# Kernel optimization log

Measured on AMD Instinct MI355X. Metric: run time of the kernel, lower is better.

Reference implementation:

```python
import jax, jax.numpy as jnp
import numpy as np

B, K, N, F, H = 20000, 10, 100000, 256, 128


def setup_inputs() -> dict:
    key = jax.random.key(0)
    ks = jax.random.split(key, 8)
    neighbors = jax.random.randint(ks[0], (B, K), 0, N)
    embed_table = jax.random.normal(ks[1], (N, F), dtype=jnp.float32)
    w = lambda k, shp: jax.random.normal(k, shp, dtype=jnp.float32) * 0.05
    return {
        "neighbors": neighbors,
        "embed_table": embed_table,
        "W1a": w(ks[2], (F, H)), "W1b": w(ks[3], (H, H)),
        "W2a": w(ks[4], (F, H)), "W2b": w(ks[5], (H, H)),
        "W3a": w(ks[6], (F, H)), "W3b": w(ks[7], (H, H)),
    }


def reference(neighbors, embed_table, W1a, W1b, W2a, W2b, W3a, W3b):
    # Gather each batch node's K sampled neighbor embeddings: [B, K, F]
    x = embed_table[neighbors]
    # Three MLP projections: Linear(F,H,no bias) -> tanh -> Linear(H,H,no bias)
    q = jnp.tanh(x @ W1a) @ W1b              # [B, K, H]  (att1)
    k = jnp.tanh(x @ W2a) @ W2b              # [B, K, H]  (att2)
    v = jnp.tanh(x @ W3a) @ W3b              # [B, K, H]  (att3)
    # Per-node attention over the K neighbors, softmax along last dim
    att = jax.nn.softmax(jnp.einsum('bid,bjd->bij', q, k), axis=-1)  # [B, K, K]
    # torch: sum over rows of (att @ v) -> contract both i and j
    out = jnp.einsum('bij,bjd->bd', att, v)  # [B, H]
    return out
```

## Files before the change

### kernel.cpp

```cpp
#include <hip/hip_runtime.h>
#include <hip/hip_bf16.h>

constexpr int B_ = 20000;
constexpr int K_ = 10;
constexpr int N_ = 100000;
constexpr int F_ = 256;
constexpr int H_ = 128;
constexpr int RW = 3 * H_;

typedef __attribute__((ext_vector_type(8))) short bf16x8;
typedef __attribute__((ext_vector_type(4))) float f32x4;

__device__ __forceinline__ unsigned short f2bf(float x) {
  unsigned int u = __builtin_bit_cast(unsigned int, x);
  unsigned int r = u + 0x7fffu + ((u >> 16) & 1u);
  return (unsigned short)(r >> 16);
}

__device__ __forceinline__ float bf2f(unsigned int u16) {
  return __builtin_bit_cast(float, u16 << 16);
}

__device__ __forceinline__ unsigned int cvt_pk_bf16(float lo, float hi) {
  unsigned int r;
  asm("v_cvt_pk_bf16_f32 %0, %1, %2" : "=v"(r) : "v"(lo), "v"(hi));
  return r;
}

__device__ __forceinline__ float fast_tanh(float x) {
  float e = __expf(2.0f * x);
  return 1.0f - 2.0f * __builtin_amdgcn_rcpf(e + 1.0f);
}

__global__ __launch_bounds__(256) void prep_kernel(
    const float* __restrict__ W1a, const float* __restrict__ W1b,
    const float* __restrict__ W2a, const float* __restrict__ W2b,
    const float* __restrict__ W3a, const float* __restrict__ W3b,
    unsigned short* __restrict__ wat2, unsigned short* __restrict__ wbt2) {
  const float* Wa[3] = {W1a, W2a, W3a};
  const float* Wb[3] = {W1b, W2b, W3b};
  int g = blockIdx.x * 256 + threadIdx.x;
  if (g < 3 * 64 * 512) {
    int chunk = g >> 9;
    int e = g & 511;
    int lane = e >> 3, j = e & 7;
    int c = chunk & 7;
    int ks = (chunk >> 3) & 7;
    int p = chunk >> 6;
    int k = 32 * ks + 8 * (lane >> 4) + j;
    int h = 16 * c + (lane & 15);
    wat2[g] = f2bf(Wa[p][k * H_ + h]);
  } else {
    int g2 = g - 3 * 64 * 512;
    int chunk = g2 >> 9;
    int e = g2 & 511;
    int lane = e >> 3, j = e & 7;
    int ks2 = chunk & 3;
    int c2 = (chunk >> 2) & 7;
    int p = chunk >> 5;
    int k = 32 * ks2 + 8 * (lane >> 4) + j;
    int h2 = 16 * c2 + (lane & 15);
    wbt2[g2] = f2bf(Wb[p][k * H_ + h2]);
  }
}

constexpr int MT = 16;
constexpr int XS = F_ + 8;
constexpr int TS = H_ + 8;

__global__ __launch_bounds__(128) void proj_kernel(
    const float* __restrict__ E,
    const unsigned short* __restrict__ wat2,
    const unsigned short* __restrict__ wbt2,
    unsigned short* __restrict__ qkvI) {
  __shared__ unsigned short xs[MT * XS];
  __shared__ unsigned short ts[MT * TS];

  const int tid = threadIdx.x;
  const int lane = tid & 63;
  const int w = tid >> 6;
  const int l15 = lane & 15;
  const int q = lane >> 4;
  const int row0 = blockIdx.x * MT;

  {
    const float4* Eg = (const float4*)E;
#pragma unroll
    for (int it = 0; it < 8; ++it) {
      int i = tid + 128 * it;
      int r = i >> 6;
      int c4 = i & 63;
      int row = row0 + r;
      if (row >= N_) row = N_ - 1;
      float4 v = Eg[(size_t)row * (F_ / 4) + c4];
      unsigned int lo = cvt_pk_bf16(v.x, v.y);
      unsigned int hi = cvt_pk_bf16(v.z, v.w);
      *(uint2*)&xs[r * XS + c4 * 4] = make_uint2(lo, hi);
    }
  }
  __syncthreads();

  for (int p = 0; p < 3; ++p) {
    const unsigned short* __restrict__ wa = wat2 + p * (64 * 512);
    const unsigned short* __restrict__ wb = wbt2 + p * (32 * 512);

    f32x4 acc[4];
#pragma unroll
    for (int i = 0; i < 4; ++i) acc[i] = (f32x4)0.0f;

#pragma unroll
    for (int ks = 0; ks < 8; ++ks) {
      bf16x8 bx = *(const bf16x8*)&xs[l15 * XS + 32 * ks + 8 * q];
#pragma unroll
      for (int i = 0; i < 4; ++i) {
        bf16x8 af = *(const bf16x8*)&wa[(ks * 8 + 4 * w + i) * 512 + lane * 8];
        acc[i] = __builtin_amdgcn_mfma_f32_16x16x32_bf16(af, bx, acc[i], 0, 0, 0);
      }
    }

    __syncthreads();
#pragma unroll
    for (int i = 0; i < 4; ++i) {
      unsigned int lo = cvt_pk_bf16(fast_tanh(acc[i][0]), fast_tanh(acc[i][1]));
      unsigned int hi = cvt_pk_bf16(fast_tanh(acc[i][2]), fast_tanh(acc[i][3]));
      *(uint2*)&ts[l15 * TS + 16 * (4 * w + i) + 4 * q] = make_uint2(lo, hi);
    }
    __syncthreads();

    f32x4 ac2[4];
#pragma unroll
    for (int i = 0; i < 4; ++i) ac2[i] = (f32x4)0.0f;

#pragma unroll
    for (int ks2 = 0; ks2 < 4; ++ks2) {
      bf16x8 bt = *(const bf16x8*)&ts[l15 * TS + 32 * ks2 + 8 * q];
#pragma unroll
      for (int i = 0; i < 4; ++i) {
        bf16x8 ab = *(const bf16x8*)&wb[((4 * w + i) * 4 + ks2) * 512 + lane * 8];
        ac2[i] = __builtin_amdgcn_mfma_f32_16x16x32_bf16(ab, bt, ac2[i], 0, 0, 0);
      }
    }

#pragma unroll
    for (int i = 0; i < 4; ++i) {
      int n = row0 + l15;
      if (n < N_) {
        unsigned int lo = cvt_pk_bf16(ac2[i][0], ac2[i][1]);
        unsigned int hi = cvt_pk_bf16(ac2[i][2], ac2[i][3]);
        *(uint2*)&qkvI[(size_t)n * RW + p * H_ + 16 * (4 * w + i) + 4 * q] =
            make_uint2(lo, hi);
      }
    }
  }
}

__global__ __launch_bounds__(256) void agg_kernel(
    const int* __restrict__ nbr,
    const unsigned short* __restrict__ qkvI,
    float* __restrict__ out) {
  const int lane = threadIdx.x & 63;
  const int wv = threadIdx.x >> 6;
  const int b = blockIdx.x * 4 + wv;
  const int l15 = lane & 15;
  const int kg = lane >> 4;

  const int ni = nbr[b * K_ + (l15 < K_ ? l15 : 0)];
  const size_t nbase = (size_t)ni * RW;

  f32x4 sc = (f32x4)0.0f;
#pragma unroll
  for (int k = 0; k < 4; ++k) {
    const int off = k * 32 + kg * 8;
    bf16x8 qf = *(const bf16x8*)&qkvI[nbase + off];
    bf16x8 kf = *(const bf16x8*)&qkvI[nbase + H_ + off];
    sc = __builtin_amdgcn_mfma_f32_16x16x32_bf16(qf, kf, sc, 0, 0, 0);
  }

  if (l15 >= K_) {
#pragma unroll
    for (int r = 0; r < 4; ++r) sc[r] = -3.0e38f;
  }

  float mx[4], e[4], sm[4];
#pragma unroll
  for (int r = 0; r < 4; ++r) mx[r] = sc[r];
#pragma unroll
  for (int st = 1; st < 16; st <<= 1)
#pragma unroll
    for (int r = 0; r < 4; ++r) mx[r] = fmaxf(mx[r], __shfl_xor(mx[r], st, 16));
#pragma unroll
  for (int r = 0; r < 4; ++r) { e[r] = __expf(sc[r] - mx[r]); sm[r] = e[r]; }
#pragma unroll
  for (int st = 1; st < 16; st <<= 1)
#pragma unroll
    for (int r = 0; r < 4; ++r) sm[r] += __shfl_xor(sm[r], st, 16);

  float cs = 0.0f;
#pragma unroll
  for (int r = 0; r < 4; ++r) {
    float a = e[r] * __builtin_amdgcn_rcpf(sm[r]);
    if (kg * 4 + r >= K_) a = 0.0f;
    cs += a;
  }
  cs += __shfl_xor(cs, 16, 64);
  cs += __shfl_xor(cs, 32, 64);

  float o0 = 0.0f, o1 = 0.0f;
#pragma unroll
  for (int j = 0; j < K_; ++j) {
    const float cj = __shfl(cs, j, 64);
    const int nj = __shfl(ni, j, 64);
    const unsigned int v2 =
        *(const unsigned int*)&qkvI[(size_t)nj * RW + 2 * H_ + 2 * lane];
    o0 = fmaf(cj, bf2f(v2 & 0xffffu), o0);
    o1 = fmaf(cj, bf2f(v2 >> 16), o1);
  }
  *(float2*)&out[(size_t)b * H_ + 2 * lane] = make_float2(o0, o1);
}

extern "C" void kernel_launch(void* const* d_in, const int* in_sizes, int n_in,
                              void* d_out, int out_size, void* d_ws, size_t ws_size,
                              hipStream_t stream) {
  const int* nbr = (const int*)d_in[0];
  const float* E = (const float*)d_in[1];
  const float* W1a = (const float*)d_in[2];
  const float* W1b = (const float*)d_in[3];
  const float* W2a = (const float*)d_in[4];
  const float* W2b = (const float*)d_in[5];
  const float* W3a = (const float*)d_in[6];
  const float* W3b = (const float*)d_in[7];
  float* out = (float*)d_out;

  unsigned short* qkvI = (unsigned short*)d_ws;
  unsigned short* wat2 = qkvI + (size_t)N_ * RW;
  unsigned short* wbt2 = wat2 + (size_t)3 * 64 * 512;

  prep_kernel<<<(3 * 64 * 512 + 3 * 32 * 512) / 256, 256, 0, stream>>>(
      W1a, W1b, W2a, W2b, W3a, W3b, wat2, wbt2);
  proj_kernel<<<(N_ + MT - 1) / MT, 128, 0, stream>>>(E, wat2, wbt2, qkvI);
  agg_kernel<<<B_ / 4, 256, 0, stream>>>(nbr, qkvI, out);
}
```

Baseline: 262.0 us.

## Tile projection over 64 rows with per-wave row ownership and private scratch

The projection kernel now handles 64 embedding rows per block with 256 threads. Each wave owns 16 rows and computes all 128 output columns, instead of two waves splitting the columns of a 16-row tile. The tanh intermediate goes to a per-wave LDS scratch, so the block-wide barriers between the two matmuls are removed. Weight fragments are reused across more rows per block, at the cost of more accumulator registers and larger LDS use, which may lower occupancy.

```diff
diff --git a/kernel.cpp b/kernel.cpp
--- a/kernel.cpp
+++ b/kernel.cpp
@@ -64,17 +64,17 @@
   }
 }
 
-constexpr int MT = 16;
+constexpr int MT = 64;
 constexpr int XS = F_ + 8;
-constexpr int TS = H_ + 8;
-
-__global__ __launch_bounds__(128) void proj_kernel(
+constexpr int SPAD = 68;
+
+__global__ __launch_bounds__(256) void proj_kernel(
     const float* __restrict__ E,
     const unsigned short* __restrict__ wat2,
     const unsigned short* __restrict__ wbt2,
     unsigned short* __restrict__ qkvI) {
   __shared__ unsigned short xs[MT * XS];
-  __shared__ unsigned short ts[MT * TS];
+  __shared__ unsigned int scr[4 * 16 * SPAD];
 
   const int tid = threadIdx.x;
   const int lane = tid & 63;
@@ -82,12 +82,13 @@
   const int l15 = lane & 15;
   const int q = lane >> 4;
   const int row0 = blockIdx.x * MT;
+  unsigned int* scw = scr + w * (16 * SPAD);
 
   {
     const float4* Eg = (const float4*)E;
 #pragma unroll
-    for (int it = 0; it < 8; ++it) {
-      int i = tid + 128 * it;
+    for (int it = 0; it < 16; ++it) {
+      int i = tid + 256 * it;
       int r = i >> 6;
       int c4 = i & 63;
       int row = row0 + r;
@@ -104,50 +105,48 @@
     const unsigned short* __restrict__ wa = wat2 + p * (64 * 512);
     const unsigned short* __restrict__ wb = wbt2 + p * (32 * 512);
 
-    f32x4 acc[4];
-#pragma unroll
-    for (int i = 0; i < 4; ++i) acc[i] = (f32x4)0.0f;
+    f32x4 acc[8];
+#pragma unroll
+    for (int hp = 0; hp < 8; ++hp) acc[hp] = (f32x4)0.0f;
 
 #pragma unroll
     for (int ks = 0; ks < 8; ++ks) {
-      bf16x8 bx = *(const bf16x8*)&xs[l15 * XS + 32 * ks + 8 * q];
-#pragma unroll
-      for (int i = 0; i < 4; ++i) {
-        bf16x8 af = *(const bf16x8*)&wa[(ks * 8 + 4 * w + i) * 512 + lane * 8];
-        acc[i] = __builtin_amdgcn_mfma_f32_16x16x32_bf16(af, bx, acc[i], 0, 0, 0);
+      bf16x8 bx = *(const bf16x8*)&xs[(16 * w + l15) * XS + 32 * ks + 8 * q];
+#pragma unroll
+      for (int hp = 0; hp < 8; ++hp) {
+        bf16x8 af = *(const bf16x8*)&wa[(ks * 8 + hp) * 512 + lane * 8];
+        acc[hp] = __builtin_amdgcn_mfma_f32_16x16x32_bf16(af, bx, acc[hp], 0, 0, 0);
       }
     }
 
-    __syncthreads();
-#pragma unroll
-    for (int i = 0; i < 4; ++i) {
-      unsigned int lo = cvt_pk_bf16(fast_tanh(acc[i][0]), fast_tanh(acc[i][1]));
-      unsigned int hi = cvt_pk_bf16(fast_tanh(acc[i][2]), fast_tanh(acc[i][3]));
-      *(uint2*)&ts[l15 * TS + 16 * (4 * w + i) + 4 * q] = make_uint2(lo, hi);
-    }
-    __syncthreads();
-
-    f32x4 ac2[4];
-#pragma unroll
-    for (int i = 0; i < 4; ++i) ac2[i] = (f32x4)0.0f;
+#pragma unroll
+    for (int hp = 0; hp < 8; ++hp) {
+      unsigned int lo = cvt_pk_bf16(fast_tanh(acc[hp][0]), fast_tanh(acc[hp][1]));
+      unsigned int hi = cvt_pk_bf16(fast_tanh(acc[hp][2]), fast_tanh(acc[hp][3]));
+      *(uint2*)&scw[l15 * SPAD + 8 * hp + 2 * q] = make_uint2(lo, hi);
+    }
+
+    f32x4 ac2[8];
+#pragma unroll
+    for (int c2 = 0; c2 < 8; ++c2) ac2[c2] = (f32x4)0.0f;
 
 #pragma unroll
     for (int ks2 = 0; ks2 < 4; ++ks2) {
-      bf16x8 bt = *(const bf16x8*)&ts[l15 * TS + 32 * ks2 + 8 * q];
-#pragma unroll
-      for (int i = 0; i < 4; ++i) {
-        bf16x8 ab = *(const bf16x8*)&wb[((4 * w + i) * 4 + ks2) * 512 + lane * 8];
-        ac2[i] = __builtin_amdgcn_mfma_f32_16x16x32_bf16(ab, bt, ac2[i], 0, 0, 0);
+      bf16x8 bt = *(const bf16x8*)&scw[l15 * SPAD + 16 * ks2 + 4 * q];
+#pragma unroll
+      for (int c2 = 0; c2 < 8; ++c2) {
+        bf16x8 ab = *(const bf16x8*)&wb[(c2 * 4 + ks2) * 512 + lane * 8];
+        ac2[c2] = __builtin_amdgcn_mfma_f32_16x16x32_bf16(ab, bt, ac2[c2], 0, 0, 0);
       }
     }
 
 #pragma unroll
-    for (int i = 0; i < 4; ++i) {
-      int n = row0 + l15;
+    for (int c2 = 0; c2 < 8; ++c2) {
+      int n = row0 + 16 * w + l15;
       if (n < N_) {
-        unsigned int lo = cvt_pk_bf16(ac2[i][0], ac2[i][1]);
-        unsigned int hi = cvt_pk_bf16(ac2[i][2], ac2[i][3]);
-        *(uint2*)&qkvI[(size_t)n * RW + p * H_ + 16 * (4 * w + i) + 4 * q] =
+        unsigned int lo = cvt_pk_bf16(ac2[c2][0], ac2[c2][1]);
+        unsigned int hi = cvt_pk_bf16(ac2[c2][2], ac2[c2][3]);
+        *(uint2*)&qkvI[(size_t)n * RW + p * H_ + 16 * c2 + 4 * q] =
             make_uint2(lo, hi);
       }
     }
@@ -237,6 +236,6 @@
 
   prep_kernel<<<(3 * 64 * 512 + 3 * 32 * 512) / 256, 256, 0, stream>>>(
       W1a, W1b, W2a, W2b, W3a, W3b, wat2, wbt2);
-  proj_kernel<<<(N_ + MT - 1) / MT, 128, 0, stream>>>(E, wat2, wbt2, qkvI);
+  proj_kernel<<<(N_ + MT - 1) / MT, 256, 0, stream>>>(E, wat2, wbt2, qkvI);
   agg_kernel<<<B_ / 4, 256, 0, stream>>>(nbr, qkvI, out);
 }
```

Result: slower. 391.3 us (+49.4%).
